# Performance work log

Measured on AMD Instinct MI355X. Metric: run time of the kernel, lower is better.

Reference implementation:

```python
import jax, jax.numpy as jnp
import numpy as np

DIM = 1024
EXP = 4           # expansion_factor
NUM_EXPERTS = 4
BATCH, SEQ = 4, 4096


def setup_inputs() -> dict:
    key = jax.random.key(0)
    ks = jax.random.split(key, 6)
    x = jax.random.normal(ks[0], (BATCH, SEQ, DIM), dtype=jnp.float32)
    token_mask = jax.random.randint(ks[1], (BATCH, SEQ), 0, NUM_EXPERTS, dtype=jnp.int32)
    hid = DIM * EXP
    s1 = 1.0 / np.sqrt(DIM)
    s2 = 1.0 / np.sqrt(hid)
    # nn.Linear layout: weight [out_features, in_features]
    w1 = jax.random.uniform(ks[2], (hid, DIM), minval=-s1, maxval=s1, dtype=jnp.float32)
    b1 = jax.random.uniform(ks[3], (hid,), minval=-s1, maxval=s1, dtype=jnp.float32)
    w2 = jax.random.uniform(ks[4], (DIM, hid), minval=-s2, maxval=s2, dtype=jnp.float32)
    b2 = jax.random.uniform(ks[5], (DIM,), minval=-s2, maxval=s2, dtype=jnp.float32)
    return {"x": x, "w1": w1, "b1": b1, "w2": w2, "b2": b2, "token_mask": token_mask}


def _nested_ffn(x, w1, b1, w2, b2, token_mask):
    dim = x.shape[-1]            # in_features of proj1
    out_dim = w2.shape[0]        # out_features of proj2 (== dim)
    # Expert m uses the first D_m = width >> (E-1-m) features (matryoshka nesting).
    # Expand (proj1): truncating input features to D_m and doing a full GEMM is
    # exactly equivalent to zeroing features >= D_m, so we mask then do one GEMM.
    d_in = dim >> (NUM_EXPERTS - 1 - token_mask)             # [B,S]
    in_mask = jnp.arange(dim) < d_in[..., None]              # [B,S,dim]
    h = jnp.einsum('bsd,fd->bsf', jnp.where(in_mask, x, jnp.zeros((), x.dtype)), w1) + b1
    h = jax.nn.gelu(h, approximate=False)                    # torch nn.GELU() default = erf
    # Contract (proj2): expert m produces only the first D_m outputs (incl. bias),
    # padded with zeros -> compute full GEMM then mask outputs.
    d_out = out_dim >> (NUM_EXPERTS - 1 - token_mask)        # [B,S]
    out_mask = jnp.arange(out_dim) < d_out[..., None]        # [B,S,out_dim]
    y = jnp.einsum('bsf,df->bsd', h, w2) + b2
    return jnp.where(out_mask, y, jnp.zeros((), y.dtype))


def reference(x, w1, b1, w2, b2, token_mask):
    return _nested_ffn(x, w1, b1, w2, b2, token_mask)
```

## Files before the change

### kernel.cpp

```cpp
#include <hip/hip_runtime.h>
#include <hip/hip_bf16.h>


typedef __bf16 bf16x8 __attribute__((ext_vector_type(8)));
typedef float f32x4 __attribute__((ext_vector_type(4)));

#define M_TOK   16384
#define DIM     1024
#define HID     4096

#define META_T     31
#define META_BLK   64
#define META_MAP   256
#define META_RT    2560

__device__ inline unsigned int pk_bf16(float a, float b) {
  unsigned int r;
  asm("v_cvt_pk_bf16_f32 %0, %1, %2" : "=v"(r) : "v"(a), "v"(b));
  return r;
}

__device__ inline float gelu_f(float v) {
  float v2 = v * v;
  float w = v * fmaf(0.10294324f, v2, 2.30220830f);
  float e = __builtin_amdgcn_exp2f(-w);
  return v * __builtin_amdgcn_rcpf(1.0f + e);
}

__device__ inline void async_copy16(const void* g, void* s) {
  __builtin_amdgcn_global_load_lds(
      (const __attribute__((address_space(1))) unsigned int*)g,
      (__attribute__((address_space(3))) unsigned int*)s,
      16, 0, 0);
}

template<int ROWS, int LDK>
__device__ inline void stage_tile(const unsigned short* __restrict__ g,
                                  int row0, int k0, char* lds) {
  const char* gbase = (const char*)g;
  int tid = threadIdx.x;
#pragma unroll
  for (int i = 0; i < ROWS / 32; ++i) {
    int q = i * 256 + tid;
    int r = q >> 3;
    int c = q & 7;
    int gc = c ^ (r & 7);
    const void* gp = gbase + ((size_t)(row0 + r) * LDK + (size_t)k0 + gc * 8) * 2;
    async_copy16(gp, lds + (size_t)q * 16);
  }
}

__global__ __launch_bounds__(1024) void sortw_kernel(
    const int* __restrict__ tm,
    const float* __restrict__ w1,
    const float* __restrict__ w2,
    int* __restrict__ meta,
    unsigned short* __restrict__ w1b,
    unsigned short* __restrict__ w2b) {
  int tid = threadIdx.x;
  if (blockIdx.x != 0) {
    size_t i = (size_t)(blockIdx.x - 1) * 4096 + tid * 4;
    const float* src;
    unsigned short* dst;
    if (i < (size_t)HID * DIM) { src = w1; dst = w1b; }
    else { src = w2 - (size_t)HID * DIM; dst = w2b - (size_t)HID * DIM; }
    float4 v = *(const float4*)(src + i);
    uint2 o;
    o.x = pk_bf16(v.x, v.y);
    o.y = pk_bf16(v.z, v.w);
    *(uint2*)(dst + i) = o;
    return;
  }

  __shared__ unsigned short rt[16384];
  __shared__ unsigned int w01[16], w23[16];
  __shared__ int sbase[4];
  __shared__ int cb[128];
  __shared__ int pfx[129];
  int lane = tid & 63, wv = tid >> 6;

  int c0 = 0, c1 = 0, c2 = 0, c3 = 0;
  unsigned int epack = 0;
  int4 tv[4];
#pragma unroll
  for (int j = 0; j < 4; ++j)
    tv[j] = *(const int4*)(tm + tid * 16 + j * 4);
#pragma unroll
  for (int j = 0; j < 4; ++j) {
    int e;
    e = tv[j].x; epack |= (unsigned)e << (2 * (4 * j + 0)); c0 += (e == 0); c1 += (e == 1); c2 += (e == 2); c3 += (e == 3);
    e = tv[j].y; epack |= (unsigned)e << (2 * (4 * j + 1)); c0 += (e == 0); c1 += (e == 1); c2 += (e == 2); c3 += (e == 3);
    e = tv[j].z; epack |= (unsigned)e << (2 * (4 * j + 2)); c0 += (e == 0); c1 += (e == 1); c2 += (e == 2); c3 += (e == 3);
    e = tv[j].w; epack |= (unsigned)e << (2 * (4 * j + 3)); c0 += (e == 0); c1 += (e == 1); c2 += (e == 2); c3 += (e == 3);
  }
  unsigned int p01 = (unsigned)c0 | ((unsigned)c1 << 16);
  unsigned int p23 = (unsigned)c2 | ((unsigned)c3 << 16);
  unsigned int i01 = p01, i23 = p23;
#pragma unroll
  for (int s = 1; s < 64; s <<= 1) {
    unsigned int t0 = __shfl_up(i01, s, 64);
    unsigned int t1 = __shfl_up(i23, s, 64);
    if (lane >= s) { i01 += t0; i23 += t1; }
  }
  if (lane == 63) { w01[wv] = i01; w23[wv] = i23; }
  unsigned int e01 = i01 - p01, e23 = i23 - p23;
  __syncthreads();
  if (tid < 16) {
    unsigned int a = w01[tid], b = w23[tid];
    unsigned int ia = a, ib = b;
#pragma unroll
    for (int s = 1; s < 16; s <<= 1) {
      unsigned int t0 = __shfl_up(ia, s, 64);
      unsigned int t1 = __shfl_up(ib, s, 64);
      if (tid >= s) { ia += t0; ib += t1; }
    }
    w01[tid] = ia - a;
    w23[tid] = ib - b;
    if (tid == 15) {
      int t0 = (int)(ia & 0xFFFF), t1 = (int)(ia >> 16), t2 = (int)(ib & 0xFFFF);
      sbase[0] = 0; sbase[1] = t0; sbase[2] = t0 + t1; sbase[3] = t0 + t1 + t2;
    }
  }
  __syncthreads();
  int off0 = sbase[0] + (int)((w01[wv] & 0xFFFF) + (e01 & 0xFFFF));
  int off1 = sbase[1] + (int)((w01[wv] >> 16) + (e01 >> 16));
  int off2 = sbase[2] + (int)((w23[wv] & 0xFFFF) + (e23 & 0xFFFF));
  int off3 = sbase[3] + (int)((w23[wv] >> 16) + (e23 >> 16));
#pragma unroll
  for (int j = 0; j < 16; ++j) {
    int e = (epack >> (2 * j)) & 3;
    int t = tid * 16 + j;
    int pos = (e == 0) ? off0++ : (e == 1) ? off1++ : (e == 2) ? off2++ : off3++;
    rt[pos] = (unsigned short)(t | (e << 14));
  }
  __syncthreads();

  if (tid < 64) {
    int s0 = tid * 2, s1 = s0 + 1;
    int l0 = s0 * 128 + 127, l1 = s1 * 128 + 127;
    int e0 = (l0 >= sbase[1]) + (l0 >= sbase[2]) + (l0 >= sbase[3]);
    int e1 = (l1 >= sbase[1]) + (l1 >= sbase[2]) + (l1 >= sbase[3]);
    int v0 = 1 << e0, v1 = 1 << e1, pair = v0 + v1;
    meta[META_BLK + s0] = 128 << e0;
    meta[META_BLK + s1] = 128 << e1;
    cb[s0] = v0; cb[s1] = v1;
    int inc = pair;
#pragma unroll
    for (int s = 1; s < 64; s <<= 1) {
      int t = __shfl_up(inc, s, 64);
      if (tid >= s) inc += t;
    }
    int excl = inc - pair;
    pfx[s0] = excl; pfx[s1] = excl + v0;
    if (tid == 63) { pfx[128] = inc; meta[META_T] = inc; }
  }
  __syncthreads();
  if (tid < 128) {
    int n = cb[tid], p = pfx[tid];
    int* map = meta + META_MAP;
    for (int c = 0; c < n; ++c) map[p + c] = tid * 8 + c;
    int zp = pfx[128] + 8 * tid - pfx[tid];
    for (int c = n; c < 8; ++c) map[zp + (c - n)] = tid * 8 + c;
  }
  int* rowtok = meta + META_RT;
#pragma unroll
  for (int j = 0; j < 16; ++j)
    rowtok[j * 1024 + tid] = (int)rt[j * 1024 + tid];
}

__global__ void prepx_kernel(const float* __restrict__ x,
                             const int* __restrict__ meta,
                             unsigned short* __restrict__ xb) {
  int b = blockIdx.x;
  int tid = threadIdx.x;
  int mt = meta[META_RT + b];
  int t = mt & 0x3FFF;
  int din = 128 << (mt >> 14);
  int kb = meta[META_BLK + (b >> 7)];
  int d = tid * 4;
  if (d < kb) {
    uint2 o; o.x = 0; o.y = 0;
    if (d < din) {
      float4 v = *(const float4*)(x + (size_t)t * DIM + d);
      o.x = pk_bf16(v.x, v.y);
      o.y = pk_bf16(v.z, v.w);
    }
    *(uint2*)(xb + (size_t)b * DIM + d) = o;
  }
}

__global__ __launch_bounds__(256) void gemm1_kernel(
    const unsigned short* __restrict__ A,
    const unsigned short* __restrict__ B,
    const float* __restrict__ bias,
    const int* __restrict__ meta,
    unsigned short* __restrict__ H)
{
  constexpr int K = DIM, N = HID;
  __shared__ char smem[32768];
  char* As = smem;
  char* Bs = smem + 16384;
  int tid = threadIdx.x;
  int lane = tid & 63, quad = lane >> 4, l15 = lane & 15;
  int wave = tid >> 6, wm = wave & 1, wn = wave >> 1;
  int rowblk = 127 - (blockIdx.x >> 5);
  int row0 = rowblk * 128, col0 = (blockIdx.x & 31) * 128;
  int kmax = meta[META_BLK + rowblk];

  int chb = (quad ^ (l15 & 7)) << 4;

  f32x4 acc[4][4] = {};

  for (int k0 = 0; k0 < kmax; k0 += 64) {
    __syncthreads();
    stage_tile<128, K>(A, row0, k0, As);
    stage_tile<128, K>(B, col0, k0, Bs);
    __syncthreads();
#pragma unroll
    for (int kk = 0; kk < 2; ++kk) {
      int xo = chb ^ (kk << 6);
      bf16x8 af[4], bg[4];
#pragma unroll
      for (int mt = 0; mt < 4; ++mt)
        af[mt] = *(const bf16x8*)(As + (wm * 64 + mt * 16 + l15) * 128 + xo);
#pragma unroll
      for (int nt = 0; nt < 4; ++nt)
        bg[nt] = *(const bf16x8*)(Bs + (wn * 64 + nt * 16 + l15) * 128 + xo);
#pragma unroll
      for (int mt = 0; mt < 4; ++mt)
#pragma unroll
        for (int nt = 0; nt < 4; ++nt)
          acc[mt][nt] = __builtin_amdgcn_mfma_f32_16x16x32_bf16(
              bg[nt], af[mt], acc[mt][nt], 0, 0, 0);
    }
  }

  int t_base = row0 + wm * 64;
  int f_base = col0 + wn * 64;
#pragma unroll
  for (int nt = 0; nt < 4; ++nt) {
    int f0 = f_base + nt * 16 + quad * 4;
    float4 bv = *(const float4*)(bias + f0);
#pragma unroll
    for (int mt = 0; mt < 4; ++mt) {
      int t = t_base + mt * 16 + l15;
      float v0 = gelu_f(acc[mt][nt][0] + bv.x);
      float v1 = gelu_f(acc[mt][nt][1] + bv.y);
      float v2 = gelu_f(acc[mt][nt][2] + bv.z);
      float v3 = gelu_f(acc[mt][nt][3] + bv.w);
      uint2 p;
      p.x = pk_bf16(v0, v1);
      p.y = pk_bf16(v2, v3);
      *(uint2*)(H + (size_t)t * N + f0) = p;
    }
  }
}

__global__ __launch_bounds__(256) void gemm2_kernel(
    const unsigned short* __restrict__ A,
    const unsigned short* __restrict__ B,
    const float* __restrict__ bias,
    const int* __restrict__ meta,
    float* __restrict__ out)
{
  constexpr int K = HID, N = DIM;
  int T = meta[META_T];
  int b = blockIdx.x;
  int mp = meta[META_MAP + b];
  int row0 = (mp >> 3) * 128, col0 = (mp & 7) * 128;
  const int* rowtok = meta + META_RT;
  int tid = threadIdx.x;

  if (b >= T) {
    float4 z = make_float4(0.f, 0.f, 0.f, 0.f);
#pragma unroll
    for (int i = 0; i < 16; ++i) {
      int idx = i * 256 + tid;
      int r = idx >> 5;
      int col = (idx & 31) * 4;
      int t = rowtok[row0 + r] & 0x3FFF;
      *(float4*)(out + (size_t)t * N + col0 + col) = z;
    }
    return;
  }

  __shared__ char smem[32768];
  char* As = smem;
  char* Bs = smem + 16384;
  int lane = tid & 63, quad = lane >> 4, l15 = lane & 15;
  int wave = tid >> 6, wm = wave & 1, wn = wave >> 1;
  int chb = (quad ^ (l15 & 7)) << 4;

  f32x4 acc[4][4] = {};

  for (int k0 = 0; k0 < K; k0 += 64) {
    __syncthreads();
    stage_tile<128, K>(A, row0, k0, As);
    stage_tile<128, K>(B, col0, k0, Bs);
    __syncthreads();
#pragma unroll
    for (int kk = 0; kk < 2; ++kk) {
      int xo = chb ^ (kk << 6);
      bf16x8 af[4], bg[4];
#pragma unroll
      for (int mt = 0; mt < 4; ++mt)
        af[mt] = *(const bf16x8*)(As + (wm * 64 + mt * 16 + l15) * 128 + xo);
#pragma unroll
      for (int nt = 0; nt < 4; ++nt)
        bg[nt] = *(const bf16x8*)(Bs + (wn * 64 + nt * 16 + l15) * 128 + xo);
#pragma unroll
      for (int mt = 0; mt < 4; ++mt)
#pragma unroll
        for (int nt = 0; nt < 4; ++nt)
          acc[mt][nt] = __builtin_amdgcn_mfma_f32_16x16x32_bf16(
              bg[nt], af[mt], acc[mt][nt], 0, 0, 0);
    }
  }

  int p_base = row0 + wm * 64;
  int d_base = col0 + wn * 64;
  float4 bv[4];
#pragma unroll
  for (int nt = 0; nt < 4; ++nt)
    bv[nt] = *(const float4*)(bias + d_base + nt * 16 + quad * 4);
#pragma unroll
  for (int mt = 0; mt < 4; ++mt) {
    int m2 = rowtok[p_base + mt * 16 + l15];
    int t = m2 & 0x3FFF;
    int dout = 128 << (m2 >> 14);
#pragma unroll
    for (int nt = 0; nt < 4; ++nt) {
      int d0 = d_base + nt * 16 + quad * 4;
      bool ok = d0 < dout;
      float4 o;
      o.x = ok ? acc[mt][nt][0] + bv[nt].x : 0.0f;
      o.y = ok ? acc[mt][nt][1] + bv[nt].y : 0.0f;
      o.z = ok ? acc[mt][nt][2] + bv[nt].z : 0.0f;
      o.w = ok ? acc[mt][nt][3] + bv[nt].w : 0.0f;
      *(float4*)(out + (size_t)t * N + d0) = o;
    }
  }
}

extern "C" void kernel_launch(void* const* d_in, const int* in_sizes, int n_in,
                              void* d_out, int out_size, void* d_ws, size_t ws_size,
                              hipStream_t stream) {
  const float* x  = (const float*)d_in[0];
  const float* w1 = (const float*)d_in[1];
  const float* b1 = (const float*)d_in[2];
  const float* w2 = (const float*)d_in[3];
  const float* b2 = (const float*)d_in[4];
  const int*   tm = (const int*)d_in[5];
  float* out = (float*)d_out;

  char* ws = (char*)d_ws;
  int* meta = (int*)ws;
  unsigned short* xb  = (unsigned short*)(ws + 131072);
  unsigned short* w1b = (unsigned short*)(ws + 33685504);
  unsigned short* w2b = (unsigned short*)(ws + 42074112);
  unsigned short* hb  = (unsigned short*)(ws + 50462720);

  sortw_kernel<<<2049, 1024, 0, stream>>>(tm, w1, w2, meta, w1b, w2b);
  prepx_kernel<<<M_TOK, 256, 0, stream>>>(x, meta, xb);
  gemm1_kernel<<<4096, 256, 0, stream>>>(xb, w1b, b1, meta, hb);
  gemm2_kernel<<<1024, 256, 0, stream>>>(hb, w2b, b2, meta, out);
}
```

Before: 328.1 us.

## Partition gemm2 tile map into eight interleaved per-XCD work lists

The tile map for the second GEMM is rebuilt as eight separate lists, one per blockIdx modulo 8, each holding the active tiles of a subset of row stripes followed by the zero-fill tiles. Each block now picks its work from the list selected by blockIdx.x & 7, so blocks that the hardware places on the same XCD share row stripes and their A-operand reuse stays in that XCD's L2. The per-list active counts replace the single global count. The catch is that the map build is now a serial loop over eight threads, and work may be spread less evenly across XCDs.

```diff
diff --git a/kernel.cpp b/kernel.cpp
--- a/kernel.cpp
+++ b/kernel.cpp
@@ -9,7 +9,7 @@
 #define DIM     1024
 #define HID     4096
 
-#define META_T     31
+#define META_TK    40
 #define META_BLK   64
 #define META_MAP   256
 #define META_RT    2560
@@ -76,7 +76,6 @@
   __shared__ unsigned int w01[16], w23[16];
   __shared__ int sbase[4];
   __shared__ int cb[128];
-  __shared__ int pfx[129];
   int lane = tid & 63, wv = tid >> 6;
 
   int c0 = 0, c1 = 0, c2 = 0, c3 = 0;
@@ -135,32 +134,26 @@
   }
   __syncthreads();
 
-  if (tid < 64) {
-    int s0 = tid * 2, s1 = s0 + 1;
-    int l0 = s0 * 128 + 127, l1 = s1 * 128 + 127;
-    int e0 = (l0 >= sbase[1]) + (l0 >= sbase[2]) + (l0 >= sbase[3]);
-    int e1 = (l1 >= sbase[1]) + (l1 >= sbase[2]) + (l1 >= sbase[3]);
-    int v0 = 1 << e0, v1 = 1 << e1, pair = v0 + v1;
-    meta[META_BLK + s0] = 128 << e0;
-    meta[META_BLK + s1] = 128 << e1;
-    cb[s0] = v0; cb[s1] = v1;
-    int inc = pair;
-#pragma unroll
-    for (int s = 1; s < 64; s <<= 1) {
-      int t = __shfl_up(inc, s, 64);
-      if (tid >= s) inc += t;
-    }
-    int excl = inc - pair;
-    pfx[s0] = excl; pfx[s1] = excl + v0;
-    if (tid == 63) { pfx[128] = inc; meta[META_T] = inc; }
+  if (tid < 128) {
+    int last = tid * 128 + 127;
+    int e = (last >= sbase[1]) + (last >= sbase[2]) + (last >= sbase[3]);
+    cb[tid] = 1 << e;
+    meta[META_BLK + tid] = 128 << e;
   }
   __syncthreads();
-  if (tid < 128) {
-    int n = cb[tid], p = pfx[tid];
-    int* map = meta + META_MAP;
-    for (int c = 0; c < n; ++c) map[p + c] = tid * 8 + c;
-    int zp = pfx[128] + 8 * tid - pfx[tid];
-    for (int c = n; c < 8; ++c) map[zp + (c - n)] = tid * 8 + c;
+  if (tid < 8) {
+    int k = tid;
+    int* map = meta + META_MAP + k * 128;
+    int Tk = 0;
+    for (int j = 0; j < 16; ++j) Tk += cb[k + 8 * j];
+    meta[META_TK + k] = Tk;
+    int pos = 0, zpos = Tk;
+    for (int j = 0; j < 16; ++j) {
+      int s = k + 8 * j;
+      int n = cb[s];
+      for (int c = 0; c < n; ++c) map[pos++] = s * 8 + c;
+      for (int c = n; c < 8; ++c) map[zpos++] = s * 8 + c;
+    }
   }
   int* rowtok = meta + META_RT;
 #pragma unroll
@@ -264,14 +257,14 @@
     float* __restrict__ out)
 {
   constexpr int K = HID, N = DIM;
-  int T = meta[META_T];
-  int b = blockIdx.x;
-  int mp = meta[META_MAP + b];
+  int Bk = blockIdx.x & 7, ord = blockIdx.x >> 3;
+  int Tk = meta[META_TK + Bk];
+  int mp = meta[META_MAP + Bk * 128 + ord];
   int row0 = (mp >> 3) * 128, col0 = (mp & 7) * 128;
   const int* rowtok = meta + META_RT;
   int tid = threadIdx.x;
 
-  if (b >= T) {
+  if (ord >= Tk) {
     float4 z = make_float4(0.f, 0.f, 0.f, 0.f);
 #pragma unroll
     for (int i = 0; i < 16; ++i) {
```

After: 324.9 us. No clear change (-1.0%).
